# Kernel tuning notes

Hardware: AMD Instinct MI355X
Metric: run time of the kernel (lower is better)

The kernel has to match this reference:

```python
import jax, jax.numpy as jnp
import numpy as np

N = 100000   # nodes
E = 1600000  # edges (avg degree 16)
K = 50       # TAGConv hops per layer


def gcn_norm(edge_index, edge_weight, num_nodes):
    # PyG gcn_norm with add_self_loops=False: D^{-1/2} A D^{-1/2},
    # degree computed at the aggregation (col) side for source_to_target flow.
    row, col = edge_index[0], edge_index[1]
    deg = jax.ops.segment_sum(edge_weight, col, num_segments=num_nodes)
    dis = jnp.where(deg > 0, deg ** -0.5, jnp.zeros_like(deg))
    return dis[row] * edge_weight * dis[col]


def tagconv(x, row, col, norm, W, b):
    # out = sum_{k=0..K} (A_hat^k x) W_k + b, W: [K+1, fin, fout]
    out0 = x @ W[0] + b

    def step(carry, Wk):
        h, acc = carry
        h = jax.ops.segment_sum(norm[:, None] * h[row], col, num_segments=N)
        return (h, acc + h @ Wk), None

    (_, out), _ = jax.lax.scan(step, (x, out0), W[1:])
    return out


def setup_inputs() -> dict:
    key = jax.random.key(0)
    ks = jax.random.split(key, 8)
    edge_index = jax.random.randint(ks[0], (2, E), 0, N)
    edge_weight = jax.random.uniform(ks[1], (E,), dtype=jnp.float32)
    c = jax.random.normal(ks[2], (N,), dtype=jnp.float32)

    def glorot(k, fin, fout):
        lim = (6.0 / (fin + fout)) ** 0.5
        return jax.random.uniform(k, (K + 1, fin, fout), jnp.float32, -lim, lim)

    W1 = glorot(ks[3], 2, 15);  b1 = jnp.zeros((15,), jnp.float32)
    W2 = glorot(ks[4], 15, 30); b2 = jnp.zeros((30,), jnp.float32)
    W3 = glorot(ks[5], 30, 15); b3 = jnp.zeros((15,), jnp.float32)
    W4 = glorot(ks[6], 15, 1);  b4 = jnp.zeros((1,), jnp.float32)
    return {"edge_index": edge_index, "edge_weight": edge_weight, "c": c, "i": 123,
            "W1": W1, "b1": b1, "W2": W2, "b2": b2,
            "W3": W3, "b3": b3, "W4": W4, "b4": b4}


def reference(edge_index, edge_weight, c, i, W1, b1, W2, b2, W3, b3, W4, b4):
    cv = jnp.zeros((N,), jnp.float32).at[i].set(1.0)
    x = jnp.stack([cv, c], axis=1)  # [N, 2]
    row, col = edge_index[0], edge_index[1]
    norm = gcn_norm(edge_index, edge_weight.astype(jnp.float32), N)
    x = jax.nn.relu(tagconv(x, row, col, norm, W1, b1))
    x = jax.nn.relu(tagconv(x, row, col, norm, W2, b2))
    x = jax.nn.relu(tagconv(x, row, col, norm, W3, b3))
    x = jax.nn.relu(tagconv(x, row, col, norm, W4, b4))
    return jnp.squeeze(x)  # [N]
```

## Files before the change

### kernel.cpp

```cpp
#include <hip/hip_runtime.h>

#define NN 100000
#define NE 1600000
#define NB_N ((NN + 255) / 256)
#define NB_E ((NE + 255) / 256)
#define NB_G ((NN + 31) / 32)


__global__ void zero_kernel(int* __restrict__ cnt) {
    int i = blockIdx.x * 256 + threadIdx.x;
    if (i < NN) cnt[i] = 0;
}

__global__ void edge_pass1(const int* __restrict__ ei, int* __restrict__ cnt,
                           int* __restrict__ rank) {
    int e = blockIdx.x * 256 + threadIdx.x;
    if (e < NE) {
        int col = ei[NE + e];
        rank[e] = atomicAdd(&cnt[col], 1);
    }
}

__global__ void scan_block(const int* __restrict__ cnt, int* __restrict__ colptr,
                           int* __restrict__ bsum) {
    __shared__ int s[256];
    int t = threadIdx.x;
    int i = blockIdx.x * 256 + t;
    int v = (i < NN) ? cnt[i] : 0;
    s[t] = v;
    __syncthreads();
    for (int off = 1; off < 256; off <<= 1) {
        int x = (t >= off) ? s[t - off] : 0;
        __syncthreads();
        s[t] += x;
        __syncthreads();
    }
    if (i < NN) colptr[i] = s[t] - v;
    if (t == 255) bsum[blockIdx.x] = s[255];
}

__global__ void scan_top(int* __restrict__ bsum, int nb) {
    __shared__ int s[512];
    int t = threadIdx.x;
    int v = (t < nb) ? bsum[t] : 0;
    s[t] = v;
    __syncthreads();
    for (int off = 1; off < 512; off <<= 1) {
        int x = (t >= off) ? s[t - off] : 0;
        __syncthreads();
        s[t] += x;
        __syncthreads();
    }
    if (t < nb) bsum[t] = s[t] - v;
}

__global__ void scan_add(int* __restrict__ colptr, const int* __restrict__ bsum) {
    int i = blockIdx.x * 256 + threadIdx.x;
    if (i < NN) colptr[i] += bsum[blockIdx.x];
    if (i == 0) colptr[NN] = NE;
}

__global__ void scatter_kernel(const int* __restrict__ ei, const float* __restrict__ ew,
                               const int* __restrict__ colptr, const int* __restrict__ rank,
                               int2* __restrict__ pairs) {
    int e = blockIdx.x * 256 + threadIdx.x;
    if (e < NE) {
        int r = ei[e], col = ei[NE + e];
        pairs[colptr[col] + rank[e]] = make_int2(r, __float_as_int(ew[e]));
    }
}

__global__ void deg_dis_kernel(const int2* __restrict__ pairs, const int* __restrict__ colptr,
                               float* __restrict__ dis) {
    int n = blockIdx.x * 256 + threadIdx.x;
    if (n < NN) {
        int e0 = colptr[n], e1 = colptr[n + 1];
        float d = 0.f;
        for (int e = e0; e < e1; e++) d += __int_as_float(pairs[e].y);
        dis[n] = d > 0.f ? (float)(1.0 / sqrt((double)d)) : 0.f;
    }
}

__global__ void rescale_kernel(int2* __restrict__ pairs, const int* __restrict__ colptr,
                               const float* __restrict__ dis) {
    int n = blockIdx.x * 256 + threadIdx.x;
    if (n < NN) {
        float dn = dis[n];
        int e0 = colptr[n], e1 = colptr[n + 1];
        for (int e = e0; e < e1; e++) {
            int2 p = pairs[e];
            pairs[e] = make_int2(p.x, __float_as_int(dis[p.x] * __int_as_float(p.y) * dn));
        }
    }
}

__global__ void build_x(const float* __restrict__ c, const int* __restrict__ ip,
                        float2* __restrict__ X1) {
    int n = blockIdx.x * 256 + threadIdx.x;
    if (n < NN) {
        float2 v;
        v.x = (n == ip[0]) ? 1.f : 0.f;
        v.y = c[n];
        X1[n] = v;
    }
}


__launch_bounds__(256)
__global__ void init_acc1(const float2* __restrict__ X1, const float* __restrict__ W1,
                          const float* __restrict__ b1, float* __restrict__ acc) {
    __shared__ float sW[30], sb[15];
    int t = threadIdx.x;
    if (t < 30) sW[t] = W1[t];
    if (t < 15) sb[t] = b1[t];
    __syncthreads();
    int n = blockIdx.x * 256 + t;
    if (n >= NN) return;
    float2 x = X1[n];
    float a[16];
#pragma unroll
    for (int j = 0; j < 15; j++) a[j] = fmaf(x.x, sW[j], fmaf(x.y, sW[15 + j], sb[j]));
    a[15] = 0.f;
    float4* o = reinterpret_cast<float4*>(acc + (size_t)n * 16);
#pragma unroll
    for (int q = 0; q < 4; q++) o[q] = make_float4(a[4*q], a[4*q+1], a[4*q+2], a[4*q+3]);
}

__launch_bounds__(256)
__global__ void step1_prop(const int2* __restrict__ pairs, const int* __restrict__ colptr,
                           const float2* __restrict__ hin, float2* __restrict__ hout) {
    int t = threadIdx.x;
    int g = t >> 3, l = t & 7;
    int n = blockIdx.x * 32 + g;
    if (n >= NN) return;
    int e0 = colptr[n], e1 = colptr[n + 1];
    float h0 = 0.f, h1 = 0.f;
    for (int e = e0 + l; e < e1; e += 8) {
        int2 p = pairs[e];
        float w = __int_as_float(p.y);
        float2 v = hin[p.x];
        h0 = fmaf(w, v.x, h0);
        h1 = fmaf(w, v.y, h1);
    }
    h0 += __shfl_xor(h0, 1); h1 += __shfl_xor(h1, 1);
    h0 += __shfl_xor(h0, 2); h1 += __shfl_xor(h1, 2);
    h0 += __shfl_xor(h0, 4); h1 += __shfl_xor(h1, 4);
    if (l == 0) hout[n] = make_float2(h0, h1);
}

__launch_bounds__(256)
__global__ void step1_acc(const int2* __restrict__ pairs, const int* __restrict__ colptr,
                          const float2* __restrict__ hin, float2* __restrict__ hout,
                          float* __restrict__ acc, const float* __restrict__ Wpair) {
    __shared__ float sWm[32], sWk[32];
    int t = threadIdx.x;
    if (t < 32) {
        int f = t >> 4, j = t & 15;
        sWm[t] = (j < 15) ? Wpair[f * 15 + j] : 0.f;
        sWk[t] = (j < 15) ? Wpair[30 + f * 15 + j] : 0.f;
    }
    __syncthreads();
    int g = t >> 3, l = t & 7;
    int n = blockIdx.x * 32 + g;
    if (n >= NN) return;
    int e0 = colptr[n], e1 = colptr[n + 1];
    float h0 = 0.f, h1 = 0.f;
    for (int e = e0 + l; e < e1; e += 8) {
        int2 p = pairs[e];
        float w = __int_as_float(p.y);
        float2 v = hin[p.x];
        h0 = fmaf(w, v.x, h0);
        h1 = fmaf(w, v.y, h1);
    }
    h0 += __shfl_xor(h0, 1); h1 += __shfl_xor(h1, 1);
    h0 += __shfl_xor(h0, 2); h1 += __shfl_xor(h1, 2);
    h0 += __shfl_xor(h0, 4); h1 += __shfl_xor(h1, 4);
    if (l == 0) hout[n] = make_float2(h0, h1);
    float2 hm = hin[n];
    int j0 = 2 * l;
    float2* ap = reinterpret_cast<float2*>(acc + (size_t)n * 16 + j0);
    float2 a = *ap;
    a.x = fmaf(h0, sWk[j0],     fmaf(h1, sWk[16 + j0],     a.x));
    a.y = fmaf(h0, sWk[j0 + 1], fmaf(h1, sWk[16 + j0 + 1], a.y));
    a.x = fmaf(hm.x, sWm[j0],     fmaf(hm.y, sWm[16 + j0],     a.x));
    a.y = fmaf(hm.x, sWm[j0 + 1], fmaf(hm.y, sWm[16 + j0 + 1], a.y));
    *ap = a;
}

__global__ void relu1(const float* __restrict__ acc, float* __restrict__ X) {
    int n = blockIdx.x * 256 + threadIdx.x;
    if (n >= NN) return;
    const float4* ip = reinterpret_cast<const float4*>(acc + (size_t)n * 16);
    float4* op = reinterpret_cast<float4*>(X + (size_t)n * 16);
#pragma unroll
    for (int q = 0; q < 4; q++) {
        float4 v = ip[q];
        v.x = fmaxf(v.x, 0.f); v.y = fmaxf(v.y, 0.f);
        v.z = fmaxf(v.z, 0.f); v.w = fmaxf(v.w, 0.f);
        if (q == 3) v.w = 0.f;
        op[q] = v;
    }
}


__launch_bounds__(256)
__global__ void init_acc2(const float* __restrict__ X, const float* __restrict__ W2,
                          const float* __restrict__ b2, float4* __restrict__ acc) {
    __shared__ float sW[480];
    __shared__ float sb[32];
    int t = threadIdx.x;
    for (int q = t; q < 480; q += 256) {
        int f = q >> 5, j = q & 31;
        sW[q] = (j < 30) ? W2[f * 30 + j] : 0.f;
    }
    if (t < 32) sb[t] = (t < 30) ? b2[t] : 0.f;
    __syncthreads();
    int n = blockIdx.x * 256 + t;
    if (n >= NN) return;
    float h[15];
#pragma unroll
    for (int f = 0; f < 15; f++) h[f] = X[(size_t)n * 16 + f];
#pragma unroll
    for (int q = 0; q < 8; q++) {
        float4 a = make_float4(sb[4*q], sb[4*q+1], sb[4*q+2], sb[4*q+3]);
#pragma unroll
        for (int f = 0; f < 15; f++) {
            float hf = h[f];
            a.x = fmaf(hf, sW[f*32 + 4*q + 0], a.x);
            a.y = fmaf(hf, sW[f*32 + 4*q + 1], a.y);
            a.z = fmaf(hf, sW[f*32 + 4*q + 2], a.z);
            a.w = fmaf(hf, sW[f*32 + 4*q + 3], a.w);
        }
        acc[(size_t)n * 8 + q] = a;
    }
}

__launch_bounds__(256)
__global__ void step2_prop(const int2* __restrict__ pairs, const int* __restrict__ colptr,
                           const float* __restrict__ hin, float* __restrict__ hout) {
    int t = threadIdx.x;
    int g = t >> 3, lane = t & 7;
    int n = blockIdx.x * 32 + g;
    if (n >= NN) return;
    float h0 = 0.f, h1 = 0.f;
    int e0 = colptr[n], e1 = colptr[n + 1];
    const float* hb = hin + 2 * lane;
    int e = e0;
    for (; e + 4 <= e1; e += 4) {
        int2 p0 = pairs[e + 0];
        int2 p1 = pairs[e + 1];
        int2 p2 = pairs[e + 2];
        int2 p3 = pairs[e + 3];
        float2 v0 = *reinterpret_cast<const float2*>(hb + (size_t)p0.x * 16);
        float2 v1 = *reinterpret_cast<const float2*>(hb + (size_t)p1.x * 16);
        float2 v2 = *reinterpret_cast<const float2*>(hb + (size_t)p2.x * 16);
        float2 v3 = *reinterpret_cast<const float2*>(hb + (size_t)p3.x * 16);
        float w0 = __int_as_float(p0.y), w1 = __int_as_float(p1.y);
        float w2 = __int_as_float(p2.y), w3 = __int_as_float(p3.y);
        h0 = fmaf(w0, v0.x, h0); h1 = fmaf(w0, v0.y, h1);
        h0 = fmaf(w1, v1.x, h0); h1 = fmaf(w1, v1.y, h1);
        h0 = fmaf(w2, v2.x, h0); h1 = fmaf(w2, v2.y, h1);
        h0 = fmaf(w3, v3.x, h0); h1 = fmaf(w3, v3.y, h1);
    }
    for (; e < e1; e++) {
        int2 p = pairs[e];
        float w = __int_as_float(p.y);
        float2 v = *reinterpret_cast<const float2*>(hb + (size_t)p.x * 16);
        h0 = fmaf(w, v.x, h0);
        h1 = fmaf(w, v.y, h1);
    }
    *reinterpret_cast<float2*>(hout + (size_t)n * 16 + 2 * lane) = make_float2(h0, h1);
}

__launch_bounds__(256)
__global__ void step2_acc(const int2* __restrict__ pairs, const int* __restrict__ colptr,
                          const float* __restrict__ hin, float* __restrict__ hout,
                          float4* __restrict__ acc, const float* __restrict__ Wpair) {
    __shared__ float sWm[480], sWk[480];
    __shared__ float shm[32][17], shk[32][17];
    int t = threadIdx.x;
    for (int q = t; q < 480; q += 256) {
        int f = q >> 5, j = q & 31;
        sWm[q] = (j < 30) ? Wpair[f * 30 + j] : 0.f;
        sWk[q] = (j < 30) ? Wpair[450 + f * 30 + j] : 0.f;
    }
    __syncthreads();
    int g = t >> 3, lane = t & 7;
    int n = blockIdx.x * 32 + g;
    if (n >= NN) return;
    float h0 = 0.f, h1 = 0.f;
    int e0 = colptr[n], e1 = colptr[n + 1];
    const float* hb = hin + 2 * lane;
    int e = e0;
    for (; e + 4 <= e1; e += 4) {
        int2 p0 = pairs[e + 0];
        int2 p1 = pairs[e + 1];
        int2 p2 = pairs[e + 2];
        int2 p3 = pairs[e + 3];
        float2 v0 = *reinterpret_cast<const float2*>(hb + (size_t)p0.x * 16);
        float2 v1 = *reinterpret_cast<const float2*>(hb + (size_t)p1.x * 16);
        float2 v2 = *reinterpret_cast<const float2*>(hb + (size_t)p2.x * 16);
        float2 v3 = *reinterpret_cast<const float2*>(hb + (size_t)p3.x * 16);
        float w0 = __int_as_float(p0.y), w1 = __int_as_float(p1.y);
        float w2 = __int_as_float(p2.y), w3 = __int_as_float(p3.y);
        h0 = fmaf(w0, v0.x, h0); h1 = fmaf(w0, v0.y, h1);
        h0 = fmaf(w1, v1.x, h0); h1 = fmaf(w1, v1.y, h1);
        h0 = fmaf(w2, v2.x, h0); h1 = fmaf(w2, v2.y, h1);
        h0 = fmaf(w3, v3.x, h0); h1 = fmaf(w3, v3.y, h1);
    }
    for (; e < e1; e++) {
        int2 p = pairs[e];
        float w = __int_as_float(p.y);
        float2 v = *reinterpret_cast<const float2*>(hb + (size_t)p.x * 16);
        h0 = fmaf(w, v.x, h0);
        h1 = fmaf(w, v.y, h1);
    }
    *reinterpret_cast<float2*>(hout + (size_t)n * 16 + 2 * lane) = make_float2(h0, h1);
    float2 hm = *reinterpret_cast<const float2*>(hin + (size_t)n * 16 + 2 * lane);
    shk[g][2 * lane] = h0;  shk[g][2 * lane + 1] = h1;
    shm[g][2 * lane] = hm.x; shm[g][2 * lane + 1] = hm.y;
    __builtin_amdgcn_wave_barrier();
    float4 a = acc[(size_t)n * 8 + lane];
#pragma unroll
    for (int f = 0; f < 15; f++) {
        float hk = shk[g][f];
        float hmf = shm[g][f];
        a.x = fmaf(hk, sWk[f*32 + 4*lane + 0], fmaf(hmf, sWm[f*32 + 4*lane + 0], a.x));
        a.y = fmaf(hk, sWk[f*32 + 4*lane + 1], fmaf(hmf, sWm[f*32 + 4*lane + 1], a.y));
        a.z = fmaf(hk, sWk[f*32 + 4*lane + 2], fmaf(hmf, sWm[f*32 + 4*lane + 2], a.z));
        a.w = fmaf(hk, sWk[f*32 + 4*lane + 3], fmaf(hmf, sWm[f*32 + 4*lane + 3], a.w));
    }
    acc[(size_t)n * 8 + lane] = a;
}

__global__ void relu2(const float4* __restrict__ acc, float4* __restrict__ X3) {
    int n = blockIdx.x * 256 + threadIdx.x;
    if (n >= NN) return;
#pragma unroll
    for (int q = 0; q < 8; q++) {
        float4 v = acc[(size_t)n * 8 + q];
        v.x = fmaxf(v.x, 0.f); v.y = fmaxf(v.y, 0.f);
        v.z = fmaxf(v.z, 0.f); v.w = fmaxf(v.w, 0.f);
        if (q == 7) { v.z = 0.f; v.w = 0.f; }
        X3[(size_t)n * 8 + q] = v;
    }
}


__launch_bounds__(256)
__global__ void init3(const float* __restrict__ X3, const float* __restrict__ Wk,
                      float* __restrict__ rout) {
    __shared__ float sW[480];
    int t = threadIdx.x;
    for (int q = t; q < 480; q += 256) {
        int f = q >> 4, j = q & 15;
        sW[q] = (j < 15) ? Wk[f * 15 + j] : 0.f;
    }
    __syncthreads();
    int n = blockIdx.x * 256 + t;
    if (n >= NN) return;
    float h[30];
#pragma unroll
    for (int f = 0; f < 30; f++) h[f] = X3[(size_t)n * 32 + f];
    float z[16];
#pragma unroll
    for (int j = 0; j < 16; j++) z[j] = 0.f;
#pragma unroll
    for (int f = 0; f < 30; f++) {
        float hf = h[f];
#pragma unroll
        for (int j = 0; j < 15; j++) z[j] = fmaf(hf, sW[f*16 + j], z[j]);
    }
    float4* o = reinterpret_cast<float4*>(rout + (size_t)n * 16);
#pragma unroll
    for (int q = 0; q < 4; q++) o[q] = make_float4(z[4*q], z[4*q+1], z[4*q+2], z[4*q+3]);
}

__launch_bounds__(256)
__global__ void step3(const int2* __restrict__ pairs, const int* __restrict__ colptr,
                      const float* __restrict__ rin, float* __restrict__ rout,
                      const float* __restrict__ h0g, const float* __restrict__ Wk) {
    __shared__ float sW[480];
    __shared__ float sh[32][33];
    int t = threadIdx.x;
    for (int q = t; q < 480; q += 256) {
        int f = q >> 4, j = q & 15;
        sW[q] = (j < 15) ? Wk[f * 15 + j] : 0.f;
    }
    __syncthreads();
    int g = t >> 3, lane = t & 7;
    int n = blockIdx.x * 32 + g;
    if (n >= NN) return;
    float4 hv = *reinterpret_cast<const float4*>(h0g + (size_t)n * 32 + 4 * lane);
    sh[g][4*lane + 0] = hv.x; sh[g][4*lane + 1] = hv.y;
    sh[g][4*lane + 2] = hv.z; sh[g][4*lane + 3] = hv.w;
    __builtin_amdgcn_wave_barrier();
    int j0 = 2 * lane;
    float z0 = 0.f, z1 = 0.f;
#pragma unroll
    for (int f = 0; f < 30; f++) {
        float hf = sh[g][f];
        z0 = fmaf(hf, sW[f*16 + j0], z0);
        z1 = fmaf(hf, sW[f*16 + j0 + 1], z1);
    }
    int e0 = colptr[n], e1 = colptr[n + 1];
    const float* rb = rin + j0;
    int e = e0;
    for (; e + 4 <= e1; e += 4) {
        int2 p0 = pairs[e + 0];
        int2 p1 = pairs[e + 1];
        int2 p2 = pairs[e + 2];
        int2 p3 = pairs[e + 3];
        float2 v0 = *reinterpret_cast<const float2*>(rb + (size_t)p0.x * 16);
        float2 v1 = *reinterpret_cast<const float2*>(rb + (size_t)p1.x * 16);
        float2 v2 = *reinterpret_cast<const float2*>(rb + (size_t)p2.x * 16);
        float2 v3 = *reinterpret_cast<const float2*>(rb + (size_t)p3.x * 16);
        float w0 = __int_as_float(p0.y), w1 = __int_as_float(p1.y);
        float w2 = __int_as_float(p2.y), w3 = __int_as_float(p3.y);
        z0 = fmaf(w0, v0.x, z0); z1 = fmaf(w0, v0.y, z1);
        z0 = fmaf(w1, v1.x, z0); z1 = fmaf(w1, v1.y, z1);
        z0 = fmaf(w2, v2.x, z0); z1 = fmaf(w2, v2.y, z1);
        z0 = fmaf(w3, v3.x, z0); z1 = fmaf(w3, v3.y, z1);
    }
    for (; e < e1; e++) {
        int2 p = pairs[e];
        float w = __int_as_float(p.y);
        float2 v = *reinterpret_cast<const float2*>(rb + (size_t)p.x * 16);
        z0 = fmaf(w, v.x, z0);
        z1 = fmaf(w, v.y, z1);
    }
    *reinterpret_cast<float2*>(rout + (size_t)n * 16 + j0) = make_float2(z0, z1);
}

__global__ void relu3(const float* __restrict__ r, const float* __restrict__ b3,
                      float* __restrict__ X4) {
    __shared__ float sb[16];
    int t = threadIdx.x;
    if (t < 16) sb[t] = (t < 15) ? b3[t] : 0.f;
    __syncthreads();
    int n = blockIdx.x * 256 + t;
    if (n >= NN) return;
#pragma unroll
    for (int j = 0; j < 16; j++) {
        float v = (j < 15) ? fmaxf(r[(size_t)n * 16 + j] + sb[j], 0.f) : 0.f;
        X4[(size_t)n * 16 + j] = v;
    }
}


__launch_bounds__(256)
__global__ void init4(const float* __restrict__ X4, const float* __restrict__ Wk,
                      float* __restrict__ rout) {
    __shared__ float sW[16];
    int t = threadIdx.x;
    if (t < 16) sW[t] = (t < 15) ? Wk[t] : 0.f;
    __syncthreads();
    int n = blockIdx.x * 256 + t;
    if (n >= NN) return;
    float z = 0.f;
#pragma unroll
    for (int f = 0; f < 15; f++) z = fmaf(X4[(size_t)n * 16 + f], sW[f], z);
    rout[n] = z;
}

__launch_bounds__(256)
__global__ void step4(const int2* __restrict__ pairs, const int* __restrict__ colptr,
                      const float* __restrict__ rin, float* __restrict__ rout,
                      const float* __restrict__ h0g, const float* __restrict__ Wk) {
    __shared__ float sW[16];
    int t = threadIdx.x;
    if (t < 16) sW[t] = (t < 15) ? Wk[t] : 0.f;
    __syncthreads();
    int g = t >> 3, l = t & 7;
    int n = blockIdx.x * 32 + g;
    if (n >= NN) return;
    int j0 = 2 * l;
    float2 xv = *reinterpret_cast<const float2*>(h0g + (size_t)n * 16 + j0);
    float z = fmaf(xv.x, sW[j0], xv.y * sW[j0 + 1]);
    int e0 = colptr[n], e1 = colptr[n + 1];
    for (int e = e0 + l; e < e1; e += 8) {
        int2 p = pairs[e];
        z = fmaf(__int_as_float(p.y), rin[p.x], z);
    }
    z += __shfl_xor(z, 1);
    z += __shfl_xor(z, 2);
    z += __shfl_xor(z, 4);
    if (l == 0) rout[n] = z;
}

__global__ void out4(const float* __restrict__ r, const float* __restrict__ b4,
                     float* __restrict__ out) {
    int n = blockIdx.x * 256 + threadIdx.x;
    if (n < NN) out[n] = fmaxf(r[n] + b4[0], 0.f);
}


extern "C" void kernel_launch(void* const* d_in, const int* in_sizes, int n_in,
                              void* d_out, int out_size, void* d_ws, size_t ws_size,
                              hipStream_t stream) {
    const int*   ei = (const int*)d_in[0];
    const float* ew = (const float*)d_in[1];
    const float* c  = (const float*)d_in[2];
    const int*   ip = (const int*)d_in[3];
    const float* W1 = (const float*)d_in[4];  const float* b1 = (const float*)d_in[5];
    const float* W2 = (const float*)d_in[6];  const float* b2 = (const float*)d_in[7];
    const float* W3 = (const float*)d_in[8];  const float* b3 = (const float*)d_in[9];
    const float* W4 = (const float*)d_in[10]; const float* b4 = (const float*)d_in[11];
    float* out = (float*)d_out;

    char* ws = (char*)d_ws;
    size_t off = 0;
    auto alloc = [&](size_t bytes) -> char* {
        char* p = ws + off;
        off = (off + bytes + 255) & ~(size_t)255;
        return p;
    };
    int2*  pairs  = (int2*)alloc((size_t)NE * 8);
    int*   colptr = (int*)alloc((size_t)(NN + 1) * 4);
    int*   bsum   = (int*)alloc(512 * 4);
    float* HA     = (float*)alloc((size_t)NN * 16 * 4);
    float* HB     = (float*)alloc((size_t)NN * 16 * 4);
    char*  accR   = alloc((size_t)NN * 32 * 4);
    char*  x3R    = alloc((size_t)NN * 32 * 4);
    char*  x4R    = alloc((size_t)NN * 16 * 4);

    float*  ACC = (float*)accR;
    float*  RA  = (float*)accR;
    float*  RB  = (float*)(accR + (size_t)NN * 4);
    float*  X3  = (float*)x3R;
    int*    rank = (int*)x3R;
    int*    cnt  = (int*)(x3R + (size_t)NE * 4);
    float*  dis  = (float*)(x3R + (size_t)NE * 4 + (size_t)NN * 4);
    float*  X4  = (float*)x4R;
    float2* X1  = (float2*)x4R;

    zero_kernel<<<NB_N, 256, 0, stream>>>(cnt);
    edge_pass1<<<NB_E, 256, 0, stream>>>(ei, cnt, rank);
    scan_block<<<NB_N, 256, 0, stream>>>(cnt, colptr, bsum);
    scan_top<<<1, 512, 0, stream>>>(bsum, NB_N);
    scan_add<<<NB_N, 256, 0, stream>>>(colptr, bsum);
    scatter_kernel<<<NB_E, 256, 0, stream>>>(ei, ew, colptr, rank, pairs);
    deg_dis_kernel<<<NB_N, 256, 0, stream>>>(pairs, colptr, dis);
    rescale_kernel<<<NB_N, 256, 0, stream>>>(pairs, colptr, dis);
    build_x<<<NB_N, 256, 0, stream>>>(c, ip, X1);

    init_acc1<<<NB_N, 256, 0, stream>>>(X1, W1, b1, ACC);
    {
        const float2* hin = X1;
        float2* hout = (float2*)HA;
        for (int k = 1; k <= 50; k++) {
            if (k & 1) {
                step1_prop<<<NB_G, 256, 0, stream>>>(pairs, colptr, hin, hout);
            } else {
                step1_acc<<<NB_G, 256, 0, stream>>>(pairs, colptr, hin, hout, ACC,
                                                    W1 + (size_t)(k - 1) * 30);
            }
            hin = hout;
            hout = (hout == (float2*)HA) ? (float2*)HB : (float2*)HA;
        }
    }
    relu1<<<NB_N, 256, 0, stream>>>(ACC, HA);

    init_acc2<<<NB_N, 256, 0, stream>>>(HA, W2, b2, (float4*)ACC);
    {
        const float* hin = HA;
        float* hout = HB;
        for (int k = 1; k <= 50; k++) {
            if (k & 1) {
                step2_prop<<<NB_G, 256, 0, stream>>>(pairs, colptr, hin, hout);
            } else {
                step2_acc<<<NB_G, 256, 0, stream>>>(pairs, colptr, hin, hout, (float4*)ACC,
                                                    W2 + (size_t)(k - 1) * 450);
            }
            const float* tp = hin; hin = hout; hout = (float*)tp;
        }
    }
    relu2<<<NB_N, 256, 0, stream>>>((const float4*)ACC, (float4*)X3);

    init3<<<NB_N, 256, 0, stream>>>(X3, W3 + (size_t)50 * 450, HA);
    {
        const float* rin = HA;
        float* rout = HB;
        for (int k = 49; k >= 0; k--) {
            step3<<<NB_G, 256, 0, stream>>>(pairs, colptr, rin, rout, X3, W3 + (size_t)k * 450);
            const float* tp = rin; rin = rout; rout = (float*)tp;
        }
        relu3<<<NB_N, 256, 0, stream>>>(rin, b3, X4);
    }

    init4<<<NB_N, 256, 0, stream>>>(X4, W4 + (size_t)50 * 15, RA);
    {
        const float* rin = RA;
        float* rout = RB;
        for (int k = 49; k >= 0; k--) {
            step4<<<NB_G, 256, 0, stream>>>(pairs, colptr, rin, rout, X4, W4 + (size_t)k * 15);
            const float* tp = rin; rin = rout; rout = (float*)tp;
        }
        out4<<<NB_N, 256, 0, stream>>>(rin, b4, out);
    }
}
```

Before: 4.040 ms.

## Split 16-wide feature arrays into two 8-wide halves for layers 2 and 3

Layers 2 and 3 now store their 16-float node feature arrays as two separate 8-float arrays. Each propagation step runs as two kernels, one per half. The intent is to shrink the per-pass gather working set to 3.2 MB so it stays resident in cache, which should make the random neighbour gathers cheaper. The cost is twice the kernel launches and twice the reads of the edge list (pairs and colptr), plus a scratch buffer that carries the layer-3 dense term from the first-half kernel to the second.

```diff
diff --git a/kernel.cpp b/kernel.cpp
--- a/kernel.cpp
+++ b/kernel.cpp
@@ -187,25 +187,23 @@
     *ap = a;
 }
 
-__global__ void relu1(const float* __restrict__ acc, float* __restrict__ X) {
+__global__ void relu1(const float* __restrict__ acc, float* __restrict__ XA,
+                      float* __restrict__ XB) {
     int n = blockIdx.x * 256 + threadIdx.x;
     if (n >= NN) return;
-    const float4* ip = reinterpret_cast<const float4*>(acc + (size_t)n * 16);
-    float4* op = reinterpret_cast<float4*>(X + (size_t)n * 16);
-#pragma unroll
-    for (int q = 0; q < 4; q++) {
-        float4 v = ip[q];
-        v.x = fmaxf(v.x, 0.f); v.y = fmaxf(v.y, 0.f);
-        v.z = fmaxf(v.z, 0.f); v.w = fmaxf(v.w, 0.f);
-        if (q == 3) v.w = 0.f;
-        op[q] = v;
-    }
-}
-
-
-__launch_bounds__(256)
-__global__ void init_acc2(const float* __restrict__ X, const float* __restrict__ W2,
-                          const float* __restrict__ b2, float4* __restrict__ acc) {
+    const float* ip = acc + (size_t)n * 16;
+#pragma unroll
+    for (int j = 0; j < 8; j++) XA[(size_t)n * 8 + j] = fmaxf(ip[j], 0.f);
+#pragma unroll
+    for (int j = 0; j < 7; j++) XB[(size_t)n * 8 + j] = fmaxf(ip[8 + j], 0.f);
+    XB[(size_t)n * 8 + 7] = 0.f;
+}
+
+
+__launch_bounds__(256)
+__global__ void init_acc2(const float* __restrict__ XA, const float* __restrict__ XB,
+                          const float* __restrict__ W2, const float* __restrict__ b2,
+                          float4* __restrict__ acc) {
     __shared__ float sW[480];
     __shared__ float sb[32];
     int t = threadIdx.x;
@@ -219,7 +217,9 @@
     if (n >= NN) return;
     float h[15];
 #pragma unroll
-    for (int f = 0; f < 15; f++) h[f] = X[(size_t)n * 16 + f];
+    for (int f = 0; f < 8; f++) h[f] = XA[(size_t)n * 8 + f];
+#pragma unroll
+    for (int f = 0; f < 7; f++) h[8 + f] = XB[(size_t)n * 8 + f];
 #pragma unroll
     for (int q = 0; q < 8; q++) {
         float4 a = make_float4(sb[4*q], sb[4*q+1], sb[4*q+2], sb[4*q+3]);
@@ -236,46 +236,42 @@
 }
 
 __launch_bounds__(256)
-__global__ void step2_prop(const int2* __restrict__ pairs, const int* __restrict__ colptr,
-                           const float* __restrict__ hin, float* __restrict__ hout) {
-    int t = threadIdx.x;
-    int g = t >> 3, lane = t & 7;
+__global__ void step_h8(const int2* __restrict__ pairs, const int* __restrict__ colptr,
+                        const float* __restrict__ hin, float* __restrict__ hout) {
+    int t = threadIdx.x;
+    int g = t >> 3, l = t & 7;
     int n = blockIdx.x * 32 + g;
     if (n >= NN) return;
-    float h0 = 0.f, h1 = 0.f;
+    float h = 0.f;
     int e0 = colptr[n], e1 = colptr[n + 1];
-    const float* hb = hin + 2 * lane;
+    const float* hb = hin + l;
     int e = e0;
     for (; e + 4 <= e1; e += 4) {
         int2 p0 = pairs[e + 0];
         int2 p1 = pairs[e + 1];
         int2 p2 = pairs[e + 2];
         int2 p3 = pairs[e + 3];
-        float2 v0 = *reinterpret_cast<const float2*>(hb + (size_t)p0.x * 16);
-        float2 v1 = *reinterpret_cast<const float2*>(hb + (size_t)p1.x * 16);
-        float2 v2 = *reinterpret_cast<const float2*>(hb + (size_t)p2.x * 16);
-        float2 v3 = *reinterpret_cast<const float2*>(hb + (size_t)p3.x * 16);
-        float w0 = __int_as_float(p0.y), w1 = __int_as_float(p1.y);
-        float w2 = __int_as_float(p2.y), w3 = __int_as_float(p3.y);
-        h0 = fmaf(w0, v0.x, h0); h1 = fmaf(w0, v0.y, h1);
-        h0 = fmaf(w1, v1.x, h0); h1 = fmaf(w1, v1.y, h1);
-        h0 = fmaf(w2, v2.x, h0); h1 = fmaf(w2, v2.y, h1);
-        h0 = fmaf(w3, v3.x, h0); h1 = fmaf(w3, v3.y, h1);
+        float v0 = hb[(size_t)p0.x * 8];
+        float v1 = hb[(size_t)p1.x * 8];
+        float v2 = hb[(size_t)p2.x * 8];
+        float v3 = hb[(size_t)p3.x * 8];
+        h = fmaf(__int_as_float(p0.y), v0, h);
+        h = fmaf(__int_as_float(p1.y), v1, h);
+        h = fmaf(__int_as_float(p2.y), v2, h);
+        h = fmaf(__int_as_float(p3.y), v3, h);
     }
     for (; e < e1; e++) {
         int2 p = pairs[e];
-        float w = __int_as_float(p.y);
-        float2 v = *reinterpret_cast<const float2*>(hb + (size_t)p.x * 16);
-        h0 = fmaf(w, v.x, h0);
-        h1 = fmaf(w, v.y, h1);
-    }
-    *reinterpret_cast<float2*>(hout + (size_t)n * 16 + 2 * lane) = make_float2(h0, h1);
-}
-
-__launch_bounds__(256)
-__global__ void step2_acc(const int2* __restrict__ pairs, const int* __restrict__ colptr,
-                          const float* __restrict__ hin, float* __restrict__ hout,
-                          float4* __restrict__ acc, const float* __restrict__ Wpair) {
+        h = fmaf(__int_as_float(p.y), hb[(size_t)p.x * 8], h);
+    }
+    hout[(size_t)n * 8 + l] = h;
+}
+
+__launch_bounds__(256)
+__global__ void step2b_acc(const int2* __restrict__ pairs, const int* __restrict__ colptr,
+                           const float* __restrict__ hinb, float* __restrict__ houtb,
+                           const float* __restrict__ houta, const float* __restrict__ hina,
+                           float4* __restrict__ acc, const float* __restrict__ Wpair) {
     __shared__ float sWm[480], sWk[480];
     __shared__ float shm[32][17], shk[32][17];
     int t = threadIdx.x;
@@ -285,52 +281,49 @@
         sWk[q] = (j < 30) ? Wpair[450 + f * 30 + j] : 0.f;
     }
     __syncthreads();
-    int g = t >> 3, lane = t & 7;
+    int g = t >> 3, l = t & 7;
     int n = blockIdx.x * 32 + g;
     if (n >= NN) return;
-    float h0 = 0.f, h1 = 0.f;
+    float h = 0.f;
     int e0 = colptr[n], e1 = colptr[n + 1];
-    const float* hb = hin + 2 * lane;
+    const float* hb = hinb + l;
     int e = e0;
     for (; e + 4 <= e1; e += 4) {
         int2 p0 = pairs[e + 0];
         int2 p1 = pairs[e + 1];
         int2 p2 = pairs[e + 2];
         int2 p3 = pairs[e + 3];
-        float2 v0 = *reinterpret_cast<const float2*>(hb + (size_t)p0.x * 16);
-        float2 v1 = *reinterpret_cast<const float2*>(hb + (size_t)p1.x * 16);
-        float2 v2 = *reinterpret_cast<const float2*>(hb + (size_t)p2.x * 16);
-        float2 v3 = *reinterpret_cast<const float2*>(hb + (size_t)p3.x * 16);
-        float w0 = __int_as_float(p0.y), w1 = __int_as_float(p1.y);
-        float w2 = __int_as_float(p2.y), w3 = __int_as_float(p3.y);
-        h0 = fmaf(w0, v0.x, h0); h1 = fmaf(w0, v0.y, h1);
-        h0 = fmaf(w1, v1.x, h0); h1 = fmaf(w1, v1.y, h1);
-        h0 = fmaf(w2, v2.x, h0); h1 = fmaf(w2, v2.y, h1);
-        h0 = fmaf(w3, v3.x, h0); h1 = fmaf(w3, v3.y, h1);
+        float v0 = hb[(size_t)p0.x * 8];
+        float v1 = hb[(size_t)p1.x * 8];
+        float v2 = hb[(size_t)p2.x * 8];
+        float v3 = hb[(size_t)p3.x * 8];
+        h = fmaf(__int_as_float(p0.y), v0, h);
+        h = fmaf(__int_as_float(p1.y), v1, h);
+        h = fmaf(__int_as_float(p2.y), v2, h);
+        h = fmaf(__int_as_float(p3.y), v3, h);
     }
     for (; e < e1; e++) {
         int2 p = pairs[e];
-        float w = __int_as_float(p.y);
-        float2 v = *reinterpret_cast<const float2*>(hb + (size_t)p.x * 16);
-        h0 = fmaf(w, v.x, h0);
-        h1 = fmaf(w, v.y, h1);
-    }
-    *reinterpret_cast<float2*>(hout + (size_t)n * 16 + 2 * lane) = make_float2(h0, h1);
-    float2 hm = *reinterpret_cast<const float2*>(hin + (size_t)n * 16 + 2 * lane);
-    shk[g][2 * lane] = h0;  shk[g][2 * lane + 1] = h1;
-    shm[g][2 * lane] = hm.x; shm[g][2 * lane + 1] = hm.y;
+        h = fmaf(__int_as_float(p.y), hb[(size_t)p.x * 8], h);
+    }
+    houtb[(size_t)n * 8 + l] = h;
+    float hka = houta[(size_t)n * 8 + l];
+    float hma = hina[(size_t)n * 8 + l];
+    float hmb = hinb[(size_t)n * 8 + l];
+    shk[g][l] = hka;     shk[g][8 + l] = h;
+    shm[g][l] = hma;     shm[g][8 + l] = hmb;
     __builtin_amdgcn_wave_barrier();
-    float4 a = acc[(size_t)n * 8 + lane];
+    float4 a = acc[(size_t)n * 8 + l];
 #pragma unroll
     for (int f = 0; f < 15; f++) {
         float hk = shk[g][f];
         float hmf = shm[g][f];
-        a.x = fmaf(hk, sWk[f*32 + 4*lane + 0], fmaf(hmf, sWm[f*32 + 4*lane + 0], a.x));
-        a.y = fmaf(hk, sWk[f*32 + 4*lane + 1], fmaf(hmf, sWm[f*32 + 4*lane + 1], a.y));
-        a.z = fmaf(hk, sWk[f*32 + 4*lane + 2], fmaf(hmf, sWm[f*32 + 4*lane + 2], a.z));
-        a.w = fmaf(hk, sWk[f*32 + 4*lane + 3], fmaf(hmf, sWm[f*32 + 4*lane + 3], a.w));
-    }
-    acc[(size_t)n * 8 + lane] = a;
+        a.x = fmaf(hk, sWk[f*32 + 4*l + 0], fmaf(hmf, sWm[f*32 + 4*l + 0], a.x));
+        a.y = fmaf(hk, sWk[f*32 + 4*l + 1], fmaf(hmf, sWm[f*32 + 4*l + 1], a.y));
+        a.z = fmaf(hk, sWk[f*32 + 4*l + 2], fmaf(hmf, sWm[f*32 + 4*l + 2], a.z));
+        a.w = fmaf(hk, sWk[f*32 + 4*l + 3], fmaf(hmf, sWm[f*32 + 4*l + 3], a.w));
+    }
+    acc[(size_t)n * 8 + l] = a;
 }
 
 __global__ void relu2(const float4* __restrict__ acc, float4* __restrict__ X3) {
@@ -349,7 +342,7 @@
 
 __launch_bounds__(256)
 __global__ void init3(const float* __restrict__ X3, const float* __restrict__ Wk,
-                      float* __restrict__ rout) {
+                      float* __restrict__ ra, float* __restrict__ rb) {
     __shared__ float sW[480];
     int t = threadIdx.x;
     for (int q = t; q < 480; q += 256) {
@@ -371,15 +364,17 @@
 #pragma unroll
         for (int j = 0; j < 15; j++) z[j] = fmaf(hf, sW[f*16 + j], z[j]);
     }
-    float4* o = reinterpret_cast<float4*>(rout + (size_t)n * 16);
-#pragma unroll
-    for (int q = 0; q < 4; q++) o[q] = make_float4(z[4*q], z[4*q+1], z[4*q+2], z[4*q+3]);
-}
-
-__launch_bounds__(256)
-__global__ void step3(const int2* __restrict__ pairs, const int* __restrict__ colptr,
-                      const float* __restrict__ rin, float* __restrict__ rout,
-                      const float* __restrict__ h0g, const float* __restrict__ Wk) {
+#pragma unroll
+    for (int q = 0; q < 8; q++) ra[(size_t)n * 8 + q] = z[q];
+#pragma unroll
+    for (int q = 0; q < 8; q++) rb[(size_t)n * 8 + q] = z[8 + q];
+}
+
+__launch_bounds__(256)
+__global__ void step3a(const int2* __restrict__ pairs, const int* __restrict__ colptr,
+                       const float* __restrict__ rina, float* __restrict__ routa,
+                       const float* __restrict__ X3, float* __restrict__ zscr,
+                       const float* __restrict__ Wk) {
     __shared__ float sW[480];
     __shared__ float sh[32][33];
     int t = threadIdx.x;
@@ -388,52 +383,81 @@
         sW[q] = (j < 15) ? Wk[f * 15 + j] : 0.f;
     }
     __syncthreads();
-    int g = t >> 3, lane = t & 7;
+    int g = t >> 3, l = t & 7;
     int n = blockIdx.x * 32 + g;
     if (n >= NN) return;
-    float4 hv = *reinterpret_cast<const float4*>(h0g + (size_t)n * 32 + 4 * lane);
-    sh[g][4*lane + 0] = hv.x; sh[g][4*lane + 1] = hv.y;
-    sh[g][4*lane + 2] = hv.z; sh[g][4*lane + 3] = hv.w;
+    float4 hv = *reinterpret_cast<const float4*>(X3 + (size_t)n * 32 + 4 * l);
+    sh[g][4*l + 0] = hv.x; sh[g][4*l + 1] = hv.y;
+    sh[g][4*l + 2] = hv.z; sh[g][4*l + 3] = hv.w;
     __builtin_amdgcn_wave_barrier();
-    int j0 = 2 * lane;
-    float z0 = 0.f, z1 = 0.f;
+    int ja = l, jb = 8 + l;
+    float za = 0.f, zb = 0.f;
 #pragma unroll
     for (int f = 0; f < 30; f++) {
         float hf = sh[g][f];
-        z0 = fmaf(hf, sW[f*16 + j0], z0);
-        z1 = fmaf(hf, sW[f*16 + j0 + 1], z1);
-    }
+        za = fmaf(hf, sW[f*16 + ja], za);
+        zb = fmaf(hf, sW[f*16 + jb], zb);
+    }
+    zscr[(size_t)n * 8 + l] = zb;
     int e0 = colptr[n], e1 = colptr[n + 1];
-    const float* rb = rin + j0;
+    const float* rbase = rina + l;
     int e = e0;
     for (; e + 4 <= e1; e += 4) {
         int2 p0 = pairs[e + 0];
         int2 p1 = pairs[e + 1];
         int2 p2 = pairs[e + 2];
         int2 p3 = pairs[e + 3];
-        float2 v0 = *reinterpret_cast<const float2*>(rb + (size_t)p0.x * 16);
-        float2 v1 = *reinterpret_cast<const float2*>(rb + (size_t)p1.x * 16);
-        float2 v2 = *reinterpret_cast<const float2*>(rb + (size_t)p2.x * 16);
-        float2 v3 = *reinterpret_cast<const float2*>(rb + (size_t)p3.x * 16);
-        float w0 = __int_as_float(p0.y), w1 = __int_as_float(p1.y);
-        float w2 = __int_as_float(p2.y), w3 = __int_as_float(p3.y);
-        z0 = fmaf(w0, v0.x, z0); z1 = fmaf(w0, v0.y, z1);
-        z0 = fmaf(w1, v1.x, z0); z1 = fmaf(w1, v1.y, z1);
-        z0 = fmaf(w2, v2.x, z0); z1 = fmaf(w2, v2.y, z1);
-        z0 = fmaf(w3, v3.x, z0); z1 = fmaf(w3, v3.y, z1);
+        float v0 = rbase[(size_t)p0.x * 8];
+        float v1 = rbase[(size_t)p1.x * 8];
+        float v2 = rbase[(size_t)p2.x * 8];
+        float v3 = rbase[(size_t)p3.x * 8];
+        za = fmaf(__int_as_float(p0.y), v0, za);
+        za = fmaf(__int_as_float(p1.y), v1, za);
+        za = fmaf(__int_as_float(p2.y), v2, za);
+        za = fmaf(__int_as_float(p3.y), v3, za);
     }
     for (; e < e1; e++) {
         int2 p = pairs[e];
-        float w = __int_as_float(p.y);
-        float2 v = *reinterpret_cast<const float2*>(rb + (size_t)p.x * 16);
-        z0 = fmaf(w, v.x, z0);
-        z1 = fmaf(w, v.y, z1);
-    }
-    *reinterpret_cast<float2*>(rout + (size_t)n * 16 + j0) = make_float2(z0, z1);
-}
-
-__global__ void relu3(const float* __restrict__ r, const float* __restrict__ b3,
-                      float* __restrict__ X4) {
+        za = fmaf(__int_as_float(p.y), rbase[(size_t)p.x * 8], za);
+    }
+    routa[(size_t)n * 8 + l] = za;
+}
+
+__launch_bounds__(256)
+__global__ void step3b(const int2* __restrict__ pairs, const int* __restrict__ colptr,
+                       const float* __restrict__ rinb, float* __restrict__ routb,
+                       const float* __restrict__ zscr) {
+    int t = threadIdx.x;
+    int g = t >> 3, l = t & 7;
+    int n = blockIdx.x * 32 + g;
+    if (n >= NN) return;
+    float z = zscr[(size_t)n * 8 + l];
+    int e0 = colptr[n], e1 = colptr[n + 1];
+    const float* rbase = rinb + l;
+    int e = e0;
+    for (; e + 4 <= e1; e += 4) {
+        int2 p0 = pairs[e + 0];
+        int2 p1 = pairs[e + 1];
+        int2 p2 = pairs[e + 2];
+        int2 p3 = pairs[e + 3];
+        float v0 = rbase[(size_t)p0.x * 8];
+        float v1 = rbase[(size_t)p1.x * 8];
+        float v2 = rbase[(size_t)p2.x * 8];
+        float v3 = rbase[(size_t)p3.x * 8];
+        z = fmaf(__int_as_float(p0.y), v0, z);
+        z = fmaf(__int_as_float(p1.y), v1, z);
+        z = fmaf(__int_as_float(p2.y), v2, z);
+        z = fmaf(__int_as_float(p3.y), v3, z);
+    }
+    for (; e < e1; e++) {
+        int2 p = pairs[e];
+        z = fmaf(__int_as_float(p.y), rbase[(size_t)p.x * 8], z);
+    }
+    routb[(size_t)n * 8 + l] = z;
+}
+
+__global__ void relu3(const float* __restrict__ ra, const float* __restrict__ rb,
+                      const float* __restrict__ b3, float* __restrict__ X4) {
     __shared__ float sb[16];
     int t = threadIdx.x;
     if (t < 16) sb[t] = (t < 15) ? b3[t] : 0.f;
@@ -441,10 +465,12 @@
     int n = blockIdx.x * 256 + t;
     if (n >= NN) return;
 #pragma unroll
-    for (int j = 0; j < 16; j++) {
-        float v = (j < 15) ? fmaxf(r[(size_t)n * 16 + j] + sb[j], 0.f) : 0.f;
-        X4[(size_t)n * 16 + j] = v;
-    }
+    for (int j = 0; j < 8; j++)
+        X4[(size_t)n * 16 + j] = fmaxf(ra[(size_t)n * 8 + j] + sb[j], 0.f);
+#pragma unroll
+    for (int j = 0; j < 7; j++)
+        X4[(size_t)n * 16 + 8 + j] = fmaxf(rb[(size_t)n * 8 + j] + sb[8 + j], 0.f);
+    X4[(size_t)n * 16 + 15] = 0.f;
 }
 
 
@@ -524,15 +550,19 @@
     char*  x3R    = alloc((size_t)NN * 32 * 4);
     char*  x4R    = alloc((size_t)NN * 16 * 4);
 
-    float*  ACC = (float*)accR;
-    float*  RA  = (float*)accR;
-    float*  RB  = (float*)(accR + (size_t)NN * 4);
-    float*  X3  = (float*)x3R;
+    float*  ACC  = (float*)accR;
+    float*  zscr = (float*)accR;
+    float*  RA   = (float*)(accR + (size_t)NN * 16);
+    float*  RB   = (float*)(accR + (size_t)NN * 20);
+    float*  X3   = (float*)x3R;
     int*    rank = (int*)x3R;
     int*    cnt  = (int*)(x3R + (size_t)NE * 4);
     float*  dis  = (float*)(x3R + (size_t)NE * 4 + (size_t)NN * 4);
-    float*  X4  = (float*)x4R;
-    float2* X1  = (float2*)x4R;
+    float*  X4   = (float*)x4R;
+    float2* X1   = (float2*)x4R;
+
+    float* HAa = HA;                 float* HAb = HA + (size_t)NN * 8;
+    float* HBa = HB;                 float* HBb = HB + (size_t)NN * 8;
 
     zero_kernel<<<NB_N, 256, 0, stream>>>(cnt);
     edge_pass1<<<NB_E, 256, 0, stream>>>(ei, cnt, rank);
@@ -559,33 +589,39 @@
             hout = (hout == (float2*)HA) ? (float2*)HB : (float2*)HA;
         }
     }
-    relu1<<<NB_N, 256, 0, stream>>>(ACC, HA);
-
-    init_acc2<<<NB_N, 256, 0, stream>>>(HA, W2, b2, (float4*)ACC);
+    relu1<<<NB_N, 256, 0, stream>>>(ACC, HAa, HAb);
+
+    init_acc2<<<NB_N, 256, 0, stream>>>(HAa, HAb, W2, b2, (float4*)ACC);
     {
-        const float* hin = HA;
-        float* hout = HB;
+        const float* hina = HAa; const float* hinb = HAb;
+        float* houta = HBa;      float* houtb = HBb;
         for (int k = 1; k <= 50; k++) {
+            step_h8<<<NB_G, 256, 0, stream>>>(pairs, colptr, hina, houta);
             if (k & 1) {
-                step2_prop<<<NB_G, 256, 0, stream>>>(pairs, colptr, hin, hout);
+                step_h8<<<NB_G, 256, 0, stream>>>(pairs, colptr, hinb, houtb);
             } else {
-                step2_acc<<<NB_G, 256, 0, stream>>>(pairs, colptr, hin, hout, (float4*)ACC,
-                                                    W2 + (size_t)(k - 1) * 450);
+                step2b_acc<<<NB_G, 256, 0, stream>>>(pairs, colptr, hinb, houtb,
+                                                     houta, hina, (float4*)ACC,
+                                                     W2 + (size_t)(k - 1) * 450);
             }
-            const float* tp = hin; hin = hout; hout = (float*)tp;
+            const float* ta = hina; hina = houta; houta = (float*)ta;
+            const float* tb = hinb; hinb = houtb; houtb = (float*)tb;
         }
     }
     relu2<<<NB_N, 256, 0, stream>>>((const float4*)ACC, (float4*)X3);
 
-    init3<<<NB_N, 256, 0, stream>>>(X3, W3 + (size_t)50 * 450, HA);
+    init3<<<NB_N, 256, 0, stream>>>(X3, W3 + (size_t)50 * 450, HAa, HAb);
     {
-        const float* rin = HA;
-        float* rout = HB;
+        const float* rina = HAa; const float* rinb = HAb;
+        float* routa = HBa;      float* routb = HBb;
         for (int k = 49; k >= 0; k--) {
-            step3<<<NB_G, 256, 0, stream>>>(pairs, colptr, rin, rout, X3, W3 + (size_t)k * 450);
-            const float* tp = rin; rin = rout; rout = (float*)tp;
+            step3a<<<NB_G, 256, 0, stream>>>(pairs, colptr, rina, routa, X3, zscr,
+                                             W3 + (size_t)k * 450);
+            step3b<<<NB_G, 256, 0, stream>>>(pairs, colptr, rinb, routb, zscr);
+            const float* ta = rina; rina = routa; routa = (float*)ta;
+            const float* tb = rinb; rinb = routb; routb = (float*)tb;
         }
-        relu3<<<NB_N, 256, 0, stream>>>(rin, b3, X4);
+        relu3<<<NB_N, 256, 0, stream>>>(rina, rinb, b3, X4);
     }
 
     init4<<<NB_N, 256, 0, stream>>>(X4, W4 + (size_t)50 * 15, RA);
```

Result: slower. 5.387 ms (+33.3%).
